# Kernel optimization log

Hardware: AMD Instinct MI355X
Metric: run time of the kernel (lower is better)

The kernel has to match this reference:

```python
import jax, jax.numpy as jnp
import numpy as np

N_NODES = 100000
N_EDGES = 1600000
F_IN, HIDDEN, N_CLASS, K = 64, 64, 32, 3
DROPOUT_P = 0.5


def setup_inputs() -> dict:
    key = jax.random.key(0)
    ks = jax.random.split(key, 5)
    x = jax.random.normal(ks[0], (N_NODES, F_IN), dtype=jnp.float32)
    edge_index = jax.random.randint(ks[1], (2, N_EDGES), 0, N_NODES, dtype=jnp.int64)
    W1 = jax.random.normal(ks[2], (K, F_IN, HIDDEN), dtype=jnp.float32) * (1.0 / np.sqrt(F_IN))
    b1 = jnp.zeros((HIDDEN,), dtype=jnp.float32)
    W2 = jax.random.normal(ks[3], (K, HIDDEN, N_CLASS), dtype=jnp.float32) * (1.0 / np.sqrt(HIDDEN))
    b2 = jnp.zeros((N_CLASS,), dtype=jnp.float32)
    return {"x": x, "edge_index": edge_index, "W1": W1, "b1": b1, "W2": W2, "b2": b2}


def _cheb_norm(edge_index, n_nodes):
    # PyG ChebConv sym norm with lambda_max=2: L_hat = -D^{-1/2} A D^{-1/2}
    row, col = edge_index[0], edge_index[1]
    deg = jax.ops.segment_sum(jnp.ones_like(row, dtype=jnp.float32), row, num_segments=n_nodes)
    dinv = jnp.where(deg > 0, jax.lax.rsqrt(jnp.maximum(deg, 1.0)), 0.0)
    return -(dinv[row] * dinv[col])  # [E]


def _cheb_conv(x, row, col, norm, W, b):
    # Chebyshev recursion: Tx0=x, Tx1=L_hat x, Tx_k = 2 L_hat Tx_{k-1} - Tx_{k-2}
    def prop(h):
        return jax.ops.segment_sum(norm[:, None] * h[col], row, num_segments=h.shape[0])
    Tx0 = x
    out = Tx0 @ W[0]
    Tx1 = prop(Tx0)
    out = out + Tx1 @ W[1]
    for k in range(2, W.shape[0]):
        Tx2 = 2.0 * prop(Tx1) - Tx0
        out = out + Tx2 @ W[k]
        Tx0, Tx1 = Tx1, Tx2
    return out + b


def reference(x, edge_index, W1, b1, W2, b2):
    row, col = edge_index[0], edge_index[1]
    norm = _cheb_norm(edge_index, x.shape[0])
    h = jax.nn.relu(_cheb_conv(x, row, col, norm, W1, b1))
    # dropout (training=True) with fixed key, inverted scaling
    keep = jax.random.bernoulli(jax.random.key(42), 1.0 - DROPOUT_P, h.shape)
    h = jnp.where(keep, h / (1.0 - DROPOUT_P), 0.0)
    out = _cheb_conv(h, row, col, norm, W2, b2)
    return jax.nn.log_softmax(out, axis=-1)
```

## Files before the change

kernel.cpp:

```cpp
#include <hip/hip_runtime.h>


static constexpr int BLK = 256;
static constexpr int SCAN_CHUNK = 256;
static constexpr int ROWB = 256;
static constexpr int RB_SHIFT = 8;
static constexpr int BCAP = 6144;
static constexpr int CHUNK = 8192;

typedef _Float16 f16x8 __attribute__((ext_vector_type(8)));
typedef _Float16 f16x2 __attribute__((ext_vector_type(2)));
typedef float f32x4 __attribute__((ext_vector_type(4)));

__device__ __forceinline__ unsigned rotl32(unsigned x, int r) {
    return (x << r) | (x >> (32 - r));
}

__device__ __forceinline__ unsigned tf_word(unsigned i) {
    const unsigned ks0 = 0u;
    const unsigned ks1 = 42u;
    const unsigned ks2 = 0u ^ 42u ^ 0x1BD11BDAu;
    unsigned x0 = 0u + ks0;
    unsigned x1 = i + ks1;
#define TF_RND(r) { x0 += x1; x1 = rotl32(x1, (r)); x1 ^= x0; }
    TF_RND(13) TF_RND(15) TF_RND(26) TF_RND(6)
    x0 += ks1; x1 += ks2 + 1u;
    TF_RND(17) TF_RND(29) TF_RND(16) TF_RND(24)
    x0 += ks2; x1 += ks0 + 2u;
    TF_RND(13) TF_RND(15) TF_RND(26) TF_RND(6)
    x0 += ks0; x1 += ks1 + 3u;
    TF_RND(17) TF_RND(29) TF_RND(16) TF_RND(24)
    x0 += ks1; x1 += ks2 + 4u;
    TF_RND(13) TF_RND(15) TF_RND(26) TF_RND(6)
    x0 += ks2; x1 += ks0 + 5u;
#undef TF_RND
    return x0 ^ x1;
}

__device__ __forceinline__ unsigned short f2h(float f) {
    union { _Float16 h; unsigned short u; } c; c.h = (_Float16)f; return c.u;
}
__device__ __forceinline__ unsigned pack2h(float a, float b) {
    union { f16x2 h; unsigned u; } c;
    c.h[0] = (_Float16)a; c.h[1] = (_Float16)b;
    return c.u;
}

__global__ void __launch_bounds__(256) k_drop(int NW, const int* __restrict__ ei,
                                              int* __restrict__ flags,
                                              unsigned long long* __restrict__ dmask) {
    if (blockIdx.x == gridDim.x - 1) {
        __shared__ int cnt_nz;
        int t = threadIdx.x;
        if (t == 0) cnt_nz = 0;
        __syncthreads();
        if (ei[2 * t + 1] != 0) atomicAdd(&cnt_nz, 1);
        __syncthreads();
        if (t == 0) flags[0] = (cnt_nz == 0) ? 1 : 0;
        return;
    }
    int idx = blockIdx.x * 256 + threadIdx.x;
    unsigned word = (idx < NW) ? tf_word((unsigned)idx) : 0u;
    unsigned long long bal = __ballot(word >> 31);
    if ((threadIdx.x & 63) == 0 && idx < NW) dmask[idx >> 6] = bal;
}

__global__ void __launch_bounds__(256) k_bin(const int* __restrict__ ei, int E,
                                             const int* __restrict__ flags,
                                             int* __restrict__ bcnt,
                                             unsigned* __restrict__ bdata, int NB) {
    __shared__ unsigned sval[CHUNK];
    __shared__ unsigned short sbkt[CHUNK];
    __shared__ int h[512], ex[512], cur[512], basep[512];
    int t = threadIdx.x;
    int start = blockIdx.x * CHUNK;
    int lim = min(CHUNK, E - start);
    bool i64 = flags[0] != 0;
    h[t] = 0; h[t + 256] = 0;
    __syncthreads();
    unsigned vv[32];
    unsigned short bb_[32];
#pragma unroll
    for (int k = 0; k < 32; ++k) {
        int idx = k * 256 + t;
        int e = start + idx;
        if (idx < lim) {
            int r, c;
            if (i64) { r = ei[2 * e]; c = ei[2 * (E + e)]; }
            else     { r = ei[e];     c = ei[E + e]; }
            int b = r >> RB_SHIFT;
            vv[k] = ((unsigned)(r & (ROWB - 1)) << 17) | (unsigned)c;
            bb_[k] = (unsigned short)b;
            atomicAdd(&h[b], 1);
        } else {
            bb_[k] = 0xFFFF;
        }
    }
    __syncthreads();
    int i0 = t, i1 = t + 256;
    ex[i0] = h[i0]; ex[i1] = h[i1];
    __syncthreads();
    for (int off = 1; off < 512; off <<= 1) {
        int v0 = (i0 >= off) ? ex[i0 - off] : 0;
        int v1 = (i1 >= off) ? ex[i1 - off] : 0;
        __syncthreads();
        ex[i0] += v0; ex[i1] += v1;
        __syncthreads();
    }
    int e0 = ex[i0] - h[i0], e1 = ex[i1] - h[i1];
    __syncthreads();
    ex[i0] = e0; cur[i0] = e0;
    ex[i1] = e1; cur[i1] = e1;
    if (i0 < NB && h[i0] > 0) basep[i0] = atomicAdd(&bcnt[i0], h[i0]);
    if (i1 < NB && h[i1] > 0) basep[i1] = atomicAdd(&bcnt[i1], h[i1]);
    __syncthreads();
#pragma unroll
    for (int k = 0; k < 32; ++k) {
        if (bb_[k] != 0xFFFF) {
            int p = atomicAdd(&cur[bb_[k]], 1);
            sval[p] = vv[k];
            sbkt[p] = bb_[k];
        }
    }
    __syncthreads();
    for (int i = t; i < lim; i += 256) {
        int b = sbkt[i];
        int gpos = basep[b] + (i - ex[b]);
        if (gpos < BCAP) bdata[(size_t)b * BCAP + gpos] = sval[i];
    }
}

__global__ void __launch_bounds__(256) k_hist2(const unsigned* __restrict__ bdata,
                                               const int* __restrict__ bcnt,
                                               int N, int* __restrict__ deg,
                                               float* __restrict__ dinv) {
    __shared__ int h[ROWB];
    int t = threadIdx.x, b = blockIdx.x;
    h[t] = 0;
    __syncthreads();
    int cnt = min(bcnt[b], BCAP);
    for (int i = t; i < cnt; i += 256)
        atomicAdd(&h[bdata[(size_t)b * BCAP + i] >> 17], 1);
    __syncthreads();
    int r = b * ROWB + t;
    if (r < N) {
        int d = h[t];
        deg[r] = d;
        dinv[r] = (d > 0) ? rsqrtf((float)d) : 0.0f;
    }
}

__global__ void k_scanA(const int* __restrict__ deg, int N, int* __restrict__ blk_sum) {
    __shared__ int lds[SCAN_CHUNK];
    int i = blockIdx.x * SCAN_CHUNK + threadIdx.x;
    int v = (i < N) ? deg[i] : 0;
    lds[threadIdx.x] = v;
    __syncthreads();
    for (int off = SCAN_CHUNK / 2; off > 0; off >>= 1) {
        if (threadIdx.x < off) lds[threadIdx.x] += lds[threadIdx.x + off];
        __syncthreads();
    }
    if (threadIdx.x == 0) blk_sum[blockIdx.x] = lds[0];
}

__global__ void k_scanB(int* __restrict__ blk_sum, int nb) {
    __shared__ int lds[1024];
    int t = threadIdx.x;
    int v = (t < nb) ? blk_sum[t] : 0;
    lds[t] = v;
    __syncthreads();
    for (int off = 1; off < 1024; off <<= 1) {
        int val = (t >= off) ? lds[t - off] : 0;
        __syncthreads();
        lds[t] += val;
        __syncthreads();
    }
    if (t < nb) blk_sum[t] = lds[t] - v;
}

__global__ void k_scanC(const int* __restrict__ deg, int N, int E,
                        const int* __restrict__ blk_sum, int* __restrict__ row_ptr) {
    __shared__ int lds[SCAN_CHUNK];
    int t = threadIdx.x;
    int i = blockIdx.x * SCAN_CHUNK + t;
    int v = (i < N) ? deg[i] : 0;
    lds[t] = v;
    __syncthreads();
    for (int off = 1; off < SCAN_CHUNK; off <<= 1) {
        int val = (t >= off) ? lds[t - off] : 0;
        __syncthreads();
        lds[t] += val;
        __syncthreads();
    }
    if (i < N) row_ptr[i] = blk_sum[blockIdx.x] + lds[t] - v;
    if (blockIdx.x == gridDim.x - 1 && t == SCAN_CHUNK - 1) row_ptr[N] = E;
}

__global__ void __launch_bounds__(256) k_place(const unsigned* __restrict__ bdata,
                                               const int* __restrict__ bcnt,
                                               const int* __restrict__ row_ptr,
                                               int N, int* __restrict__ sdst) {
    __shared__ int cur[ROWB];
    __shared__ int staged[BCAP];
    int t = threadIdx.x, b = blockIdx.x;
    int r0 = b * ROWB;
    int rbase = row_ptr[r0];
    int r = r0 + t;
    cur[t] = (r < N) ? (row_ptr[r] - rbase) : 0;
    __syncthreads();
    int cnt = min(bcnt[b], BCAP);
    for (int i = t; i < cnt; i += 256) {
        unsigned val = bdata[(size_t)b * BCAP + i];
        int p = atomicAdd(&cur[val >> 17], 1);
        staged[p] = (int)(val & 0x1FFFFu);
    }
    __syncthreads();
    for (int i = t; i < cnt; i += 256) sdst[rbase + i] = staged[i];
}

__global__ void k_wprep(const float* __restrict__ W1, const float* __restrict__ W2,
                        unsigned short* __restrict__ wt1,
                        unsigned short* __restrict__ wt2) {
    int idx = blockIdx.x * 256 + threadIdx.x;
    if (idx < 12288) {
        int c = idx >> 6, r6 = idx & 63;
        int slot = (r6 >> 3) ^ (c & 7);
        int k = slot * 8 + (r6 & 7);
        float v;
        if (c < 64)       v = W1[k * 64 + c] - W1[8192 + k * 64 + c];
        else if (c < 128) v = W1[4096 + k * 64 + (c - 64)];
        else              v = W1[8192 + k * 64 + (c - 128)];
        wt1[idx] = f2h(v);
    } else {
        int j = idx - 12288;
        int c = j >> 6, r6 = j & 63;
        int slot = (r6 >> 3) ^ (c & 7);
        int k = slot * 8 + (r6 & 7);
        float v;
        if (c < 32)      v = W2[k * 32 + c] - W2[4096 + k * 32 + c];
        else if (c < 64) v = W2[2048 + k * 32 + (c - 32)];
        else             v = W2[4096 + k * 32 + (c - 64)];
        wt2[j] = f2h(v);
    }
}

__global__ void __launch_bounds__(512) k_dense3(const float* __restrict__ x,
                                                const unsigned short* __restrict__ wt1,
                                                const float* __restrict__ b1,
                                                const float* __restrict__ dinv,
                                                int N,
                                                unsigned short* __restrict__ B16,
                                                unsigned short* __restrict__ C16,
                                                unsigned short* __restrict__ D16) {
    __shared__ unsigned short lds[20480] __attribute__((aligned(16)));
    __shared__ float sb[64];
    int t = threadIdx.x;
    int v0 = blockIdx.x * 128;
    {
        const uint4* src = (const uint4*)wt1;
        uint4* dst = (uint4*)&lds[8192];
        for (int i = t; i < 1536; i += 512) dst[i] = src[i];
    }
    if (t < 64) sb[t] = b1[t];
    {
        int row = t >> 2, c0 = (t & 3) << 4;
        int v = min(v0 + row, N - 1);
        const float* xp = x + (size_t)v * 64 + c0;
        float4 f0 = *(const float4*)xp;
        float4 f1 = *(const float4*)(xp + 4);
        float4 f2 = *(const float4*)(xp + 8);
        float4 f3 = *(const float4*)(xp + 12);
        int key = row & 7;
        int s0 = c0 >> 3;
        f16x8 h0, h1;
        h0[0] = (_Float16)f0.x; h0[1] = (_Float16)f0.y;
        h0[2] = (_Float16)f0.z; h0[3] = (_Float16)f0.w;
        h0[4] = (_Float16)f1.x; h0[5] = (_Float16)f1.y;
        h0[6] = (_Float16)f1.z; h0[7] = (_Float16)f1.w;
        h1[0] = (_Float16)f2.x; h1[1] = (_Float16)f2.y;
        h1[2] = (_Float16)f2.z; h1[3] = (_Float16)f2.w;
        h1[4] = (_Float16)f3.x; h1[5] = (_Float16)f3.y;
        h1[6] = (_Float16)f3.z; h1[7] = (_Float16)f3.w;
        *(f16x8*)&lds[row * 64 + ((s0 ^ key) << 3)] = h0;
        *(f16x8*)&lds[row * 64 + (((s0 + 1) ^ key) << 3)] = h1;
    }
    __syncthreads();

    int w = t >> 6, l = t & 63;
    int lr = l & 15, lk = l >> 4;
    int key = lr & 7;
    int arow = w * 16 + lr;
    f16x8 a0 = *(const f16x8*)&lds[arow * 64 + (((0 + lk) ^ key) << 3)];
    f16x8 a1 = *(const f16x8*)&lds[arow * 64 + (((4 + lk) ^ key) << 3)];
    f32x4 acc[12];
#pragma unroll
    for (int i = 0; i < 12; ++i) acc[i] = (f32x4){0.0f, 0.0f, 0.0f, 0.0f};
#pragma unroll
    for (int nt = 0; nt < 12; ++nt) {
        int bc = nt * 16 + lr;
        const unsigned short* wb = &lds[8192 + bc * 64];
        f16x8 b0 = *(const f16x8*)&wb[((0 + lk) ^ key) << 3];
        f16x8 b1v = *(const f16x8*)&wb[((4 + lk) ^ key) << 3];
        acc[nt] = __builtin_amdgcn_mfma_f32_16x16x32_f16(a0, b0, acc[nt], 0, 0, 0);
        acc[nt] = __builtin_amdgcn_mfma_f32_16x16x32_f16(a1, b1v, acc[nt], 0, 0, 0);
    }
    float4 dv4 = *(const float4*)&dinv[v0 + w * 16 + lk * 4];
    float dsc[4] = {dv4.x, dv4.y, dv4.z, dv4.w};
    __syncthreads();
#pragma unroll
    for (int nt = 0; nt < 4; ++nt) {
        int col = nt * 16 + lr;
        float bv = sb[col];
#pragma unroll
        for (int r = 0; r < 4; ++r) {
            int vloc = w * 16 + lk * 4 + r;
            lds[vloc * 64 + col] = f2h(acc[nt][r] + bv);
        }
    }
    __syncthreads();
#pragma unroll
    for (int q = 0; q < 2; ++q) {
        int i = q * 512 + t;
        int row = i >> 3, ch = i & 7;
        int v = v0 + row;
        if (v < N) *(uint4*)(D16 + (size_t)v * 64 + ch * 8) = ((const uint4*)lds)[i];
    }
    __syncthreads();
#pragma unroll
    for (int nt = 4; nt < 8; ++nt) {
        int col = (nt - 4) * 16 + lr;
#pragma unroll
        for (int r = 0; r < 4; ++r) {
            int vloc = w * 16 + lk * 4 + r;
            lds[vloc * 128 + col] = f2h(acc[nt][r]);
        }
    }
#pragma unroll
    for (int nt = 8; nt < 12; ++nt) {
        int col = (nt - 4) * 16 + lr;
#pragma unroll
        for (int r = 0; r < 4; ++r) {
            int vloc = w * 16 + lk * 4 + r;
            lds[vloc * 128 + col] = f2h(acc[nt][r] * dsc[r]);
        }
    }
    __syncthreads();
#pragma unroll
    for (int q = 0; q < 4; ++q) {
        int i = q * 512 + t;
        int row = i >> 4, ch = i & 15;
        int v = v0 + row;
        if (v < N) {
            uint4 val = *(const uint4*)&lds[i * 8];
            unsigned short* dst = (ch < 8)
                ? (B16 + (size_t)v * 64 + ch * 8)
                : (C16 + (size_t)v * 64 + (ch - 8) * 8);
            *(uint4*)dst = val;
        }
    }
}

__global__ void __launch_bounds__(512) k_dense3b(const unsigned short* __restrict__ wt2,
                                                 const float* __restrict__ dinv,
                                                 int N,
                                                 unsigned short* __restrict__ B16,
                                                 const unsigned short* __restrict__ C16h,
                                                 float* __restrict__ P0,
                                                 unsigned short* __restrict__ P1h) {
    __shared__ unsigned short lds[14336] __attribute__((aligned(16)));
    int t = threadIdx.x;
    int v0 = blockIdx.x * 128;
    {
        const uint4* src = (const uint4*)wt2;
        uint4* dst = (uint4*)&lds[8192];
        for (int i = t; i < 768; i += 512) dst[i] = src[i];
    }
    {
        int row = t >> 2, s0 = (t & 3) * 2;
        int v = min(v0 + row, N - 1);
        const uint4* cp = (const uint4*)(C16h + (size_t)v * 64);
        uint4 u0 = cp[s0];
        uint4 u1 = cp[s0 + 1];
        int key = row & 7;
        *(uint4*)&lds[row * 64 + ((s0 ^ key) << 3)] = u0;
        *(uint4*)&lds[row * 64 + (((s0 + 1) ^ key) << 3)] = u1;
    }
    __syncthreads();

    int w = t >> 6, l = t & 63;
    int lr = l & 15, lk = l >> 4;
    int key = lr & 7;
    int arow = w * 16 + lr;
    f16x8 a0 = *(const f16x8*)&lds[arow * 64 + (((0 + lk) ^ key) << 3)];
    f16x8 a1 = *(const f16x8*)&lds[arow * 64 + (((4 + lk) ^ key) << 3)];
    f32x4 acc[6];
#pragma unroll
    for (int i = 0; i < 6; ++i) acc[i] = (f32x4){0.0f, 0.0f, 0.0f, 0.0f};
#pragma unroll
    for (int nt = 0; nt < 6; ++nt) {
        int bc = nt * 16 + lr;
        const unsigned short* wb = &lds[8192 + bc * 64];
        f16x8 b0 = *(const f16x8*)&wb[((0 + lk) ^ key) << 3];
        f16x8 b1v = *(const f16x8*)&wb[((4 + lk) ^ key) << 3];
        acc[nt] = __builtin_amdgcn_mfma_f32_16x16x32_f16(a0, b0, acc[nt], 0, 0, 0);
        acc[nt] = __builtin_amdgcn_mfma_f32_16x16x32_f16(a1, b1v, acc[nt], 0, 0, 0);
    }
    float4 dv4 = *(const float4*)&dinv[v0 + w * 16 + lk * 4];
    float dsc[4] = {dv4.x, dv4.y, dv4.z, dv4.w};
#pragma unroll
    for (int nt = 0; nt < 2; ++nt) {
        int col = nt * 16 + lr;
#pragma unroll
        for (int r = 0; r < 4; ++r) {
            int v = v0 + w * 16 + lk * 4 + r;
            if (v < N) P0[(size_t)v * 32 + col] = acc[nt][r];
        }
    }
    __syncthreads();
#pragma unroll
    for (int nt = 2; nt < 4; ++nt) {
        int col = (nt - 2) * 16 + lr;
#pragma unroll
        for (int r = 0; r < 4; ++r) {
            int vloc = w * 16 + lk * 4 + r;
            lds[vloc * 64 + col] = f2h(acc[nt][r]);
        }
    }
#pragma unroll
    for (int nt = 4; nt < 6; ++nt) {
        int col = (nt - 2) * 16 + lr;
#pragma unroll
        for (int r = 0; r < 4; ++r) {
            int vloc = w * 16 + lk * 4 + r;
            lds[vloc * 64 + col] = f2h(acc[nt][r] * dsc[r]);
        }
    }
    __syncthreads();
#pragma unroll
    for (int q = 0; q < 2; ++q) {
        int i = q * 512 + t;
        int row = i >> 3, ch = i & 7;
        int v = v0 + row;
        if (v < N) {
            uint4 val = ((const uint4*)lds)[i];
            unsigned short* dst = (ch < 4)
                ? (P1h + (size_t)v * 32 + ch * 8)
                : (B16 + (size_t)v * 32 + (ch - 4) * 8);
            *(uint4*)dst = val;
        }
    }
}

template <int PITCH, int LPN>
__device__ __forceinline__ void gatherH(const unsigned short* __restrict__ src,
                                        const int* __restrict__ sdst,
                                        int beg, int end, int grp, int fl,
                                        float a[8]) {
    constexpr int NG = LPN / (PITCH / 8);
    f16x8 acc;
#pragma unroll
    for (int q = 0; q < 8; ++q) acc[q] = (_Float16)0;
    int e = beg + grp;
    for (; e + 3 * NG < end; e += 4 * NG) {
        int c0 = sdst[e];
        int c1 = sdst[e + NG];
        int c2 = sdst[e + 2 * NG];
        int c3 = sdst[e + 3 * NG];
        f16x8 r0 = *(const f16x8*)(src + (size_t)c0 * PITCH + 8 * fl);
        f16x8 r1 = *(const f16x8*)(src + (size_t)c1 * PITCH + 8 * fl);
        f16x8 r2 = *(const f16x8*)(src + (size_t)c2 * PITCH + 8 * fl);
        f16x8 r3 = *(const f16x8*)(src + (size_t)c3 * PITCH + 8 * fl);
        acc = acc + r0;
        acc = acc + r1;
        acc = acc + r2;
        acc = acc + r3;
    }
    for (; e < end; e += NG) {
        int c = sdst[e];
        f16x8 r = *(const f16x8*)(src + (size_t)c * PITCH + 8 * fl);
        acc = acc + r;
    }
#pragma unroll
    for (int m = PITCH / 8; m < LPN; m <<= 1) {
        union { f16x8 h; int i4[4]; } u;
        u.h = acc;
#pragma unroll
        for (int q = 0; q < 4; ++q) u.i4[q] = __shfl_xor(u.i4[q], m);
        acc = acc + u.h;
    }
#pragma unroll
    for (int q = 0; q < 8; ++q) a[q] = (float)acc[q];
}

__global__ void __launch_bounds__(BLK) k_gath1(const unsigned short* __restrict__ C16,
                                               unsigned short* __restrict__ B16,
                                               const float* __restrict__ dinv,
                                               const int* __restrict__ row_ptr,
                                               const int* __restrict__ sdst,
                                               int N) {
    int v = blockIdx.x * 16 + (threadIdx.x >> 4);
    if (v >= N) return;
    int ln = threadIdx.x & 15;
    int grp = ln >> 3, fl = ln & 7;
    float a[8];
    gatherH<64, 16>(C16, sdst, row_ptr[v], row_ptr[v + 1], grp, fl, a);
    if (grp == 0) {
        float di = dinv[v];
        float dv = -2.0f * di;
        unsigned short* p = B16 + (size_t)v * 64 + 8 * fl;
        f16x8 b = *(const f16x8*)p;
        uint4 o;
        o.x = pack2h(di * fmaf(dv, a[0], (float)b[0]), di * fmaf(dv, a[1], (float)b[1]));
        o.y = pack2h(di * fmaf(dv, a[2], (float)b[2]), di * fmaf(dv, a[3], (float)b[3]));
        o.z = pack2h(di * fmaf(dv, a[4], (float)b[4]), di * fmaf(dv, a[5], (float)b[5]));
        o.w = pack2h(di * fmaf(dv, a[6], (float)b[6]), di * fmaf(dv, a[7], (float)b[7]));
        *(uint4*)p = o;
    }
}

__global__ void __launch_bounds__(BLK) k_gath2(const unsigned short* __restrict__ D16,
                                               const unsigned short* __restrict__ B16,
                                               unsigned short* __restrict__ C16h,
                                               const unsigned long long* __restrict__ dmask,
                                               const float* __restrict__ dinv,
                                               const int* __restrict__ row_ptr,
                                               const int* __restrict__ sdst,
                                               int N) {
    int v = blockIdx.x * 16 + (threadIdx.x >> 4);
    if (v >= N) return;
    int ln = threadIdx.x & 15;
    int grp = ln >> 3, fl = ln & 7;
    float a[8];
    gatherH<64, 16>(B16, sdst, row_ptr[v], row_ptr[v + 1], grp, fl, a);
    if (grp == 0) {
        unsigned long long dm = dmask[v] >> (8 * fl);
        float dv = -dinv[v];
        f16x8 d = *(const f16x8*)(D16 + (size_t)v * 64 + 8 * fl);
        float o[8];
#pragma unroll
        for (int k = 0; k < 8; ++k)
            o[k] = fmaxf(fmaf(dv, a[k], (float)d[k]), 0.0f);
#pragma unroll
        for (int k = 0; k < 8; ++k)
            o[k] = ((dm >> k) & 1ull) ? 0.0f : o[k] * 2.0f;
        uint4 oo;
        oo.x = pack2h(o[0], o[1]); oo.y = pack2h(o[2], o[3]);
        oo.z = pack2h(o[4], o[5]); oo.w = pack2h(o[6], o[7]);
        *(uint4*)(C16h + (size_t)v * 64 + 8 * fl) = oo;
    }
}

__global__ void __launch_bounds__(BLK) k_gath3(const unsigned short* __restrict__ B16,
                                               const unsigned short* __restrict__ P1h,
                                               unsigned short* __restrict__ R16,
                                               const float* __restrict__ dinv,
                                               const int* __restrict__ row_ptr,
                                               const int* __restrict__ sdst,
                                               int N) {
    int v = blockIdx.x * 32 + (threadIdx.x >> 3);
    if (v >= N) return;
    int ln = threadIdx.x & 7;
    int grp = ln >> 2, fl = ln & 3;
    float a[8];
    gatherH<32, 8>(B16, sdst, row_ptr[v], row_ptr[v + 1], grp, fl, a);
    if (grp == 0) {
        float di = dinv[v];
        float dv = -2.0f * di;
        f16x8 d = *(const f16x8*)(P1h + (size_t)v * 32 + 8 * fl);
        uint4 o;
        o.x = pack2h(di * fmaf(dv, a[0], (float)d[0]), di * fmaf(dv, a[1], (float)d[1]));
        o.y = pack2h(di * fmaf(dv, a[2], (float)d[2]), di * fmaf(dv, a[3], (float)d[3]));
        o.z = pack2h(di * fmaf(dv, a[4], (float)d[4]), di * fmaf(dv, a[5], (float)d[5]));
        o.w = pack2h(di * fmaf(dv, a[6], (float)d[6]), di * fmaf(dv, a[7], (float)d[7]));
        *(uint4*)(R16 + (size_t)v * 32 + 8 * fl) = o;
    }
}

__global__ void __launch_bounds__(BLK) k_gath4(const unsigned short* __restrict__ R16,
                                               const float* __restrict__ P0,
                                               const float* __restrict__ dinv,
                                               const int* __restrict__ row_ptr,
                                               const int* __restrict__ sdst,
                                               const float* __restrict__ b2,
                                               int N, float* __restrict__ out) {
    int v = blockIdx.x * 32 + (threadIdx.x >> 3);
    if (v >= N) return;
    int ln = threadIdx.x & 7;
    int grp = ln >> 2, fl = ln & 3;
    float a[8];
    gatherH<32, 8>(R16, sdst, row_ptr[v], row_ptr[v + 1], grp, fl, a);
    float dv = -dinv[v];
    const float* dp = P0 + (size_t)v * 32 + 8 * fl;
    float4 dA = *(const float4*)dp;
    float4 dB = *(const float4*)(dp + 4);
    const float* bp = b2 + 8 * fl;
    float4 bA = *(const float4*)bp;
    float4 bB = *(const float4*)(bp + 4);
    float o[8];
    o[0] = fmaf(dv, a[0], dA.x + bA.x);
    o[1] = fmaf(dv, a[1], dA.y + bA.y);
    o[2] = fmaf(dv, a[2], dA.z + bA.z);
    o[3] = fmaf(dv, a[3], dA.w + bA.w);
    o[4] = fmaf(dv, a[4], dB.x + bB.x);
    o[5] = fmaf(dv, a[5], dB.y + bB.y);
    o[6] = fmaf(dv, a[6], dB.z + bB.z);
    o[7] = fmaf(dv, a[7], dB.w + bB.w);
    float m = o[0];
#pragma unroll
    for (int k = 1; k < 8; ++k) m = fmaxf(m, o[k]);
    m = fmaxf(m, __shfl_xor(m, 1));
    m = fmaxf(m, __shfl_xor(m, 2));
    float s = 0.0f;
#pragma unroll
    for (int k = 0; k < 8; ++k) s += __expf(o[k] - m);
    s += __shfl_xor(s, 1);
    s += __shfl_xor(s, 2);
    float lse = m + __logf(s);
    if (grp == 0) {
        float* op = out + (size_t)v * 32 + 8 * fl;
        *(float4*)op = make_float4(o[0] - lse, o[1] - lse, o[2] - lse, o[3] - lse);
        *(float4*)(op + 4) = make_float4(o[4] - lse, o[5] - lse, o[6] - lse, o[7] - lse);
    }
}

extern "C" void kernel_launch(void* const* d_in, const int* in_sizes, int n_in,
                              void* d_out, int out_size, void* d_ws, size_t ws_size,
                              hipStream_t stream) {
    const float* x  = (const float*)d_in[0];
    const int* ei   = (const int*)d_in[1];
    const float* W1 = (const float*)d_in[2];
    const float* b1 = (const float*)d_in[3];
    const float* W2 = (const float*)d_in[4];
    const float* b2 = (const float*)d_in[5];
    float* out = (float*)d_out;

    const int N = in_sizes[0] / 64;
    const int E = in_sizes[1] / 2;
    const int NB = (N + ROWB - 1) >> RB_SHIFT;

    char* ws = (char*)d_ws;
    size_t off = 0;
    auto alloc = [&](size_t bytes) -> void* {
        void* p = ws + off;
        off = (off + bytes + 511) & ~(size_t)511;
        return p;
    };
    int*      flags   = (int*)alloc(16);
    int*      deg     = (int*)alloc((size_t)N * 4);
    float*    dinv    = (float*)alloc((size_t)N * 4);
    int*      row_ptr = (int*)alloc(((size_t)N + 1) * 4);
    int*      blk_sum = (int*)alloc(4096);
    int*      bcnt    = (int*)alloc((size_t)NB * 4);
    size_t dbytes = (size_t)N * 64 * 4;
    size_t bdbytes = (size_t)NB * BCAP * 4;
    unsigned* bdata = (unsigned*)alloc(dbytes > bdbytes ? dbytes : bdbytes);
    unsigned short* D16 = (unsigned short*)bdata;
    float*    P0    = (float*)bdata;
    unsigned short* P1h = (unsigned short*)((char*)bdata + (size_t)N * 32 * 4);
    int*      sdst  = (int*)alloc((size_t)E * 4);
    unsigned short* C16h = (unsigned short*)alloc((size_t)N * 64 * 2);
    unsigned short* B16 = (unsigned short*)alloc((size_t)N * 64 * 2);
    unsigned short* C16 = (unsigned short*)alloc((size_t)N * 64 * 2);
    unsigned short* R16 = C16;
    unsigned long long* dmask = (unsigned long long*)alloc((size_t)N * 8);
    unsigned short* wt1 = (unsigned short*)alloc(12288 * 2);
    unsigned short* wt2 = (unsigned short*)alloc(6144 * 2);

    hipMemsetAsync(bcnt, 0, (size_t)NB * 4, stream);

    const int gW16 = (N + 15) / 16;
    const int gW32 = (N + 31) / 32;
    const int gDM = (N + 127) / 128;
    const int nb = (N + SCAN_CHUNK - 1) / SCAN_CHUNK;
    const int gBin = (E + CHUNK - 1) / CHUNK;
    const int gDrop = (N * 64 + 255) / 256;

    k_wprep<<<72, 256, 0, stream>>>(W1, W2, wt1, wt2);
    k_drop<<<gDrop + 1, 256, 0, stream>>>(N * 64, ei, flags, dmask);
    k_bin<<<gBin, 256, 0, stream>>>(ei, E, flags, bcnt, bdata, NB);
    k_hist2<<<NB, 256, 0, stream>>>(bdata, bcnt, N, deg, dinv);
    k_scanA<<<nb, SCAN_CHUNK, 0, stream>>>(deg, N, blk_sum);
    k_scanB<<<1, 1024, 0, stream>>>(blk_sum, nb);
    k_scanC<<<nb, SCAN_CHUNK, 0, stream>>>(deg, N, E, blk_sum, row_ptr);
    k_place<<<NB, 256, 0, stream>>>(bdata, bcnt, row_ptr, N, sdst);

    k_dense3<<<gDM, 512, 0, stream>>>(x, wt1, b1, dinv, N, B16, C16, D16);
    k_gath1<<<gW16, BLK, 0, stream>>>(C16, B16, dinv, row_ptr, sdst, N);
    k_gath2<<<gW16, BLK, 0, stream>>>(D16, B16, C16h, dmask, dinv, row_ptr, sdst, N);

    k_dense3b<<<gDM, 512, 0, stream>>>(wt2, dinv, N, B16, C16h, P0, P1h);
    k_gath3<<<gW32, BLK, 0, stream>>>(B16, P1h, R16, dinv, row_ptr, sdst, N);
    k_gath4<<<gW32, BLK, 0, stream>>>(R16, P0, dinv, row_ptr, sdst, b2, N, out);
}
```

Baseline: 274.7 us.

## Degree-sort nodes for gather load balance and fuse scan/init kernels

Adds a counting-sort permutation of nodes by (clamped) degree and makes all four gather kernels process nodes in that order, so the lanes of a wavefront handle rows of similar length and spend less time waiting on divergent loops. The degree scan is folded into k_hist2 (block sums) and k_place (in-block scan), removing the scanA/scanC kernels, and weight prep is merged with the dropout-mask kernel. The cost is an extra permutation kernel and an indirect perm load, plus scattered output writes and row_ptr reads that lose locality.

```diff
diff --git a/kernel.cpp b/kernel.cpp
--- a/kernel.cpp
+++ b/kernel.cpp
@@ -2,7 +2,6 @@
 
 
 static constexpr int BLK = 256;
-static constexpr int SCAN_CHUNK = 256;
 static constexpr int ROWB = 256;
 static constexpr int RB_SHIFT = 8;
 static constexpr int BCAP = 6144;
@@ -46,12 +45,25 @@
     return c.u;
 }
 
-__global__ void __launch_bounds__(256) k_drop(int NW, const int* __restrict__ ei,
+__global__ void __launch_bounds__(256) k_init(int NW, const int* __restrict__ ei,
+                                              const float* __restrict__ W1,
+                                              const float* __restrict__ W2,
                                               int* __restrict__ flags,
-                                              unsigned long long* __restrict__ dmask) {
-    if (blockIdx.x == gridDim.x - 1) {
+                                              unsigned long long* __restrict__ dmask,
+                                              unsigned short* __restrict__ wt1,
+                                              unsigned short* __restrict__ wt2,
+                                              int gDrop) {
+    int b = blockIdx.x;
+    int t = threadIdx.x;
+    if (b < gDrop) {
+        int idx = b * 256 + t;
+        unsigned word = (idx < NW) ? tf_word((unsigned)idx) : 0u;
+        unsigned long long bal = __ballot(word >> 31);
+        if ((t & 63) == 0 && idx < NW) dmask[idx >> 6] = bal;
+        return;
+    }
+    if (b == gDrop) {
         __shared__ int cnt_nz;
-        int t = threadIdx.x;
         if (t == 0) cnt_nz = 0;
         __syncthreads();
         if (ei[2 * t + 1] != 0) atomicAdd(&cnt_nz, 1);
@@ -59,169 +71,7 @@
         if (t == 0) flags[0] = (cnt_nz == 0) ? 1 : 0;
         return;
     }
-    int idx = blockIdx.x * 256 + threadIdx.x;
-    unsigned word = (idx < NW) ? tf_word((unsigned)idx) : 0u;
-    unsigned long long bal = __ballot(word >> 31);
-    if ((threadIdx.x & 63) == 0 && idx < NW) dmask[idx >> 6] = bal;
-}
-
-__global__ void __launch_bounds__(256) k_bin(const int* __restrict__ ei, int E,
-                                             const int* __restrict__ flags,
-                                             int* __restrict__ bcnt,
-                                             unsigned* __restrict__ bdata, int NB) {
-    __shared__ unsigned sval[CHUNK];
-    __shared__ unsigned short sbkt[CHUNK];
-    __shared__ int h[512], ex[512], cur[512], basep[512];
-    int t = threadIdx.x;
-    int start = blockIdx.x * CHUNK;
-    int lim = min(CHUNK, E - start);
-    bool i64 = flags[0] != 0;
-    h[t] = 0; h[t + 256] = 0;
-    __syncthreads();
-    unsigned vv[32];
-    unsigned short bb_[32];
-#pragma unroll
-    for (int k = 0; k < 32; ++k) {
-        int idx = k * 256 + t;
-        int e = start + idx;
-        if (idx < lim) {
-            int r, c;
-            if (i64) { r = ei[2 * e]; c = ei[2 * (E + e)]; }
-            else     { r = ei[e];     c = ei[E + e]; }
-            int b = r >> RB_SHIFT;
-            vv[k] = ((unsigned)(r & (ROWB - 1)) << 17) | (unsigned)c;
-            bb_[k] = (unsigned short)b;
-            atomicAdd(&h[b], 1);
-        } else {
-            bb_[k] = 0xFFFF;
-        }
-    }
-    __syncthreads();
-    int i0 = t, i1 = t + 256;
-    ex[i0] = h[i0]; ex[i1] = h[i1];
-    __syncthreads();
-    for (int off = 1; off < 512; off <<= 1) {
-        int v0 = (i0 >= off) ? ex[i0 - off] : 0;
-        int v1 = (i1 >= off) ? ex[i1 - off] : 0;
-        __syncthreads();
-        ex[i0] += v0; ex[i1] += v1;
-        __syncthreads();
-    }
-    int e0 = ex[i0] - h[i0], e1 = ex[i1] - h[i1];
-    __syncthreads();
-    ex[i0] = e0; cur[i0] = e0;
-    ex[i1] = e1; cur[i1] = e1;
-    if (i0 < NB && h[i0] > 0) basep[i0] = atomicAdd(&bcnt[i0], h[i0]);
-    if (i1 < NB && h[i1] > 0) basep[i1] = atomicAdd(&bcnt[i1], h[i1]);
-    __syncthreads();
-#pragma unroll
-    for (int k = 0; k < 32; ++k) {
-        if (bb_[k] != 0xFFFF) {
-            int p = atomicAdd(&cur[bb_[k]], 1);
-            sval[p] = vv[k];
-            sbkt[p] = bb_[k];
-        }
-    }
-    __syncthreads();
-    for (int i = t; i < lim; i += 256) {
-        int b = sbkt[i];
-        int gpos = basep[b] + (i - ex[b]);
-        if (gpos < BCAP) bdata[(size_t)b * BCAP + gpos] = sval[i];
-    }
-}
-
-__global__ void __launch_bounds__(256) k_hist2(const unsigned* __restrict__ bdata,
-                                               const int* __restrict__ bcnt,
-                                               int N, int* __restrict__ deg,
-                                               float* __restrict__ dinv) {
-    __shared__ int h[ROWB];
-    int t = threadIdx.x, b = blockIdx.x;
-    h[t] = 0;
-    __syncthreads();
-    int cnt = min(bcnt[b], BCAP);
-    for (int i = t; i < cnt; i += 256)
-        atomicAdd(&h[bdata[(size_t)b * BCAP + i] >> 17], 1);
-    __syncthreads();
-    int r = b * ROWB + t;
-    if (r < N) {
-        int d = h[t];
-        deg[r] = d;
-        dinv[r] = (d > 0) ? rsqrtf((float)d) : 0.0f;
-    }
-}
-
-__global__ void k_scanA(const int* __restrict__ deg, int N, int* __restrict__ blk_sum) {
-    __shared__ int lds[SCAN_CHUNK];
-    int i = blockIdx.x * SCAN_CHUNK + threadIdx.x;
-    int v = (i < N) ? deg[i] : 0;
-    lds[threadIdx.x] = v;
-    __syncthreads();
-    for (int off = SCAN_CHUNK / 2; off > 0; off >>= 1) {
-        if (threadIdx.x < off) lds[threadIdx.x] += lds[threadIdx.x + off];
-        __syncthreads();
-    }
-    if (threadIdx.x == 0) blk_sum[blockIdx.x] = lds[0];
-}
-
-__global__ void k_scanB(int* __restrict__ blk_sum, int nb) {
-    __shared__ int lds[1024];
-    int t = threadIdx.x;
-    int v = (t < nb) ? blk_sum[t] : 0;
-    lds[t] = v;
-    __syncthreads();
-    for (int off = 1; off < 1024; off <<= 1) {
-        int val = (t >= off) ? lds[t - off] : 0;
-        __syncthreads();
-        lds[t] += val;
-        __syncthreads();
-    }
-    if (t < nb) blk_sum[t] = lds[t] - v;
-}
-
-__global__ void k_scanC(const int* __restrict__ deg, int N, int E,
-                        const int* __restrict__ blk_sum, int* __restrict__ row_ptr) {
-    __shared__ int lds[SCAN_CHUNK];
-    int t = threadIdx.x;
-    int i = blockIdx.x * SCAN_CHUNK + t;
-    int v = (i < N) ? deg[i] : 0;
-    lds[t] = v;
-    __syncthreads();
-    for (int off = 1; off < SCAN_CHUNK; off <<= 1) {
-        int val = (t >= off) ? lds[t - off] : 0;
-        __syncthreads();
-        lds[t] += val;
-        __syncthreads();
-    }
-    if (i < N) row_ptr[i] = blk_sum[blockIdx.x] + lds[t] - v;
-    if (blockIdx.x == gridDim.x - 1 && t == SCAN_CHUNK - 1) row_ptr[N] = E;
-}
-
-__global__ void __launch_bounds__(256) k_place(const unsigned* __restrict__ bdata,
-                                               const int* __restrict__ bcnt,
-                                               const int* __restrict__ row_ptr,
-                                               int N, int* __restrict__ sdst) {
-    __shared__ int cur[ROWB];
-    __shared__ int staged[BCAP];
-    int t = threadIdx.x, b = blockIdx.x;
-    int r0 = b * ROWB;
-    int rbase = row_ptr[r0];
-    int r = r0 + t;
-    cur[t] = (r < N) ? (row_ptr[r] - rbase) : 0;
-    __syncthreads();
-    int cnt = min(bcnt[b], BCAP);
-    for (int i = t; i < cnt; i += 256) {
-        unsigned val = bdata[(size_t)b * BCAP + i];
-        int p = atomicAdd(&cur[val >> 17], 1);
-        staged[p] = (int)(val & 0x1FFFFu);
-    }
-    __syncthreads();
-    for (int i = t; i < cnt; i += 256) sdst[rbase + i] = staged[i];
-}
-
-__global__ void k_wprep(const float* __restrict__ W1, const float* __restrict__ W2,
-                        unsigned short* __restrict__ wt1,
-                        unsigned short* __restrict__ wt2) {
-    int idx = blockIdx.x * 256 + threadIdx.x;
+    int idx = (b - gDrop - 1) * 256 + t;
     if (idx < 12288) {
         int c = idx >> 6, r6 = idx & 63;
         int slot = (r6 >> 3) ^ (c & 7);
@@ -242,6 +92,169 @@
         else             v = W2[4096 + k * 32 + (c - 64)];
         wt2[j] = f2h(v);
     }
+}
+
+__global__ void __launch_bounds__(256) k_bin(const int* __restrict__ ei, int E,
+                                             const int* __restrict__ flags,
+                                             int* __restrict__ bcnt,
+                                             unsigned* __restrict__ bdata, int NB) {
+    __shared__ unsigned sval[CHUNK];
+    __shared__ unsigned short sbkt[CHUNK];
+    __shared__ int h[512], ex[512], cur[512], basep[512];
+    int t = threadIdx.x;
+    int start = blockIdx.x * CHUNK;
+    int lim = min(CHUNK, E - start);
+    bool i64 = flags[0] != 0;
+    h[t] = 0; h[t + 256] = 0;
+    __syncthreads();
+    unsigned vv[32];
+    unsigned short bb_[32];
+#pragma unroll
+    for (int k = 0; k < 32; ++k) {
+        int idx = k * 256 + t;
+        int e = start + idx;
+        if (idx < lim) {
+            int r, c;
+            if (i64) { r = ei[2 * e]; c = ei[2 * (E + e)]; }
+            else     { r = ei[e];     c = ei[E + e]; }
+            int b = r >> RB_SHIFT;
+            vv[k] = ((unsigned)(r & (ROWB - 1)) << 17) | (unsigned)c;
+            bb_[k] = (unsigned short)b;
+            atomicAdd(&h[b], 1);
+        } else {
+            bb_[k] = 0xFFFF;
+        }
+    }
+    __syncthreads();
+    int i0 = t, i1 = t + 256;
+    ex[i0] = h[i0]; ex[i1] = h[i1];
+    __syncthreads();
+    for (int off = 1; off < 512; off <<= 1) {
+        int v0 = (i0 >= off) ? ex[i0 - off] : 0;
+        int v1 = (i1 >= off) ? ex[i1 - off] : 0;
+        __syncthreads();
+        ex[i0] += v0; ex[i1] += v1;
+        __syncthreads();
+    }
+    int e0 = ex[i0] - h[i0], e1 = ex[i1] - h[i1];
+    __syncthreads();
+    ex[i0] = e0; cur[i0] = e0;
+    ex[i1] = e1; cur[i1] = e1;
+    if (i0 < NB && h[i0] > 0) basep[i0] = atomicAdd(&bcnt[i0], h[i0]);
+    if (i1 < NB && h[i1] > 0) basep[i1] = atomicAdd(&bcnt[i1], h[i1]);
+    __syncthreads();
+#pragma unroll
+    for (int k = 0; k < 32; ++k) {
+        if (bb_[k] != 0xFFFF) {
+            int p = atomicAdd(&cur[bb_[k]], 1);
+            sval[p] = vv[k];
+            sbkt[p] = bb_[k];
+        }
+    }
+    __syncthreads();
+    for (int i = t; i < lim; i += 256) {
+        int b = sbkt[i];
+        int gpos = basep[b] + (i - ex[b]);
+        if (gpos < BCAP) bdata[(size_t)b * BCAP + gpos] = sval[i];
+    }
+}
+
+__global__ void __launch_bounds__(256) k_hist2(const unsigned* __restrict__ bdata,
+                                               const int* __restrict__ bcnt,
+                                               int N, int* __restrict__ deg,
+                                               float* __restrict__ dinv,
+                                               int* __restrict__ blk_sum,
+                                               int* __restrict__ dhist) {
+    __shared__ int h[ROWB];
+    int t = threadIdx.x, b = blockIdx.x;
+    h[t] = 0;
+    __syncthreads();
+    int cnt = min(bcnt[b], BCAP);
+    for (int i = t; i < cnt; i += 256)
+        atomicAdd(&h[bdata[(size_t)b * BCAP + i] >> 17], 1);
+    __syncthreads();
+    int r = b * ROWB + t;
+    int d = h[t];
+    if (r < N) {
+        deg[r] = d;
+        dinv[r] = (d > 0) ? rsqrtf((float)d) : 0.0f;
+        atomicAdd(&dhist[min(d, 127)], 1);
+    }
+    __syncthreads();
+    for (int off = 128; off > 0; off >>= 1) {
+        if (t < off) h[t] += h[t + off];
+        __syncthreads();
+    }
+    if (t == 0) blk_sum[b] = h[0];
+}
+
+__global__ void k_scanB(int* __restrict__ blk_sum, int nb, int* __restrict__ dhist) {
+    __shared__ int lds[1024];
+    __shared__ int dl[128];
+    int t = threadIdx.x;
+    int v = (t < nb) ? blk_sum[t] : 0;
+    lds[t] = v;
+    int dv = 0;
+    if (t < 128) { dv = dhist[t]; dl[t] = dv; }
+    __syncthreads();
+    for (int off = 1; off < 1024; off <<= 1) {
+        int val = (t >= off) ? lds[t - off] : 0;
+        int dval = (t < 128 && t >= off) ? dl[t - off] : 0;
+        __syncthreads();
+        lds[t] += val;
+        if (t < 128) dl[t] += dval;
+        __syncthreads();
+    }
+    if (t < nb) blk_sum[t] = lds[t] - v;
+    if (t < 128) dhist[t] = dl[t] - dv;
+}
+
+__global__ void __launch_bounds__(256) k_perm(const int* __restrict__ deg, int N,
+                                              int* __restrict__ dhist,
+                                              int* __restrict__ perm) {
+    int v = blockIdx.x * 256 + threadIdx.x;
+    if (v < N) {
+        int d = min(deg[v], 127);
+        int pos = atomicAdd(&dhist[d], 1);
+        perm[pos] = v;
+    }
+}
+
+__global__ void __launch_bounds__(256) k_place(const unsigned* __restrict__ bdata,
+                                               const int* __restrict__ bcnt,
+                                               const int* __restrict__ deg,
+                                               const int* __restrict__ blk_sum,
+                                               int N, int E,
+                                               int* __restrict__ row_ptr,
+                                               int* __restrict__ sdst) {
+    __shared__ int cur[ROWB];
+    __shared__ int sc[ROWB];
+    __shared__ int staged[BCAP];
+    int t = threadIdx.x, b = blockIdx.x;
+    int r = b * ROWB + t;
+    int d = (r < N) ? deg[r] : 0;
+    sc[t] = d;
+    __syncthreads();
+    for (int off = 1; off < ROWB; off <<= 1) {
+        int val = (t >= off) ? sc[t - off] : 0;
+        __syncthreads();
+        sc[t] += val;
+        __syncthreads();
+    }
+    int excl = sc[t] - d;
+    int rbase = blk_sum[b];
+    if (r < N) row_ptr[r] = rbase + excl;
+    if (b == gridDim.x - 1 && t == ROWB - 1) row_ptr[N] = E;
+    cur[t] = excl;
+    __syncthreads();
+    int cnt = min(bcnt[b], BCAP);
+    for (int i = t; i < cnt; i += 256) {
+        unsigned val = bdata[(size_t)b * BCAP + i];
+        int p = atomicAdd(&cur[val >> 17], 1);
+        staged[p] = (int)(val & 0x1FFFFu);
+    }
+    __syncthreads();
+    for (int i = t; i < cnt; i += 256) sdst[rbase + i] = staged[i];
 }
 
 __global__ void __launch_bounds__(512) k_dense3(const float* __restrict__ x,
@@ -497,9 +510,11 @@
                                                const float* __restrict__ dinv,
                                                const int* __restrict__ row_ptr,
                                                const int* __restrict__ sdst,
+                                               const int* __restrict__ perm,
                                                int N) {
-    int v = blockIdx.x * 16 + (threadIdx.x >> 4);
-    if (v >= N) return;
+    int vidx = blockIdx.x * 16 + (threadIdx.x >> 4);
+    if (vidx >= N) return;
+    int v = perm[vidx];
     int ln = threadIdx.x & 15;
     int grp = ln >> 3, fl = ln & 7;
     float a[8];
@@ -525,9 +540,11 @@
                                                const float* __restrict__ dinv,
                                                const int* __restrict__ row_ptr,
                                                const int* __restrict__ sdst,
+                                               const int* __restrict__ perm,
                                                int N) {
-    int v = blockIdx.x * 16 + (threadIdx.x >> 4);
-    if (v >= N) return;
+    int vidx = blockIdx.x * 16 + (threadIdx.x >> 4);
+    if (vidx >= N) return;
+    int v = perm[vidx];
     int ln = threadIdx.x & 15;
     int grp = ln >> 3, fl = ln & 7;
     float a[8];
@@ -556,9 +573,11 @@
                                                const float* __restrict__ dinv,
                                                const int* __restrict__ row_ptr,
                                                const int* __restrict__ sdst,
+                                               const int* __restrict__ perm,
                                                int N) {
-    int v = blockIdx.x * 32 + (threadIdx.x >> 3);
-    if (v >= N) return;
+    int vidx = blockIdx.x * 32 + (threadIdx.x >> 3);
+    if (vidx >= N) return;
+    int v = perm[vidx];
     int ln = threadIdx.x & 7;
     int grp = ln >> 2, fl = ln & 3;
     float a[8];
@@ -581,10 +600,12 @@
                                                const float* __restrict__ dinv,
                                                const int* __restrict__ row_ptr,
                                                const int* __restrict__ sdst,
+                                               const int* __restrict__ perm,
                                                const float* __restrict__ b2,
                                                int N, float* __restrict__ out) {
-    int v = blockIdx.x * 32 + (threadIdx.x >> 3);
-    if (v >= N) return;
+    int vidx = blockIdx.x * 32 + (threadIdx.x >> 3);
+    if (vidx >= N) return;
+    int v = perm[vidx];
     int ln = threadIdx.x & 7;
     int grp = ln >> 2, fl = ln & 3;
     float a[8];
@@ -650,7 +671,9 @@
     float*    dinv    = (float*)alloc((size_t)N * 4);
     int*      row_ptr = (int*)alloc(((size_t)N + 1) * 4);
     int*      blk_sum = (int*)alloc(4096);
-    int*      bcnt    = (int*)alloc((size_t)NB * 4);
+    int*      bcnt    = (int*)alloc((size_t)NB * 4 + 512);
+    int*      dhist   = bcnt + NB;
+    int*      perm    = (int*)alloc((size_t)N * 4);
     size_t dbytes = (size_t)N * 64 * 4;
     size_t bdbytes = (size_t)NB * BCAP * 4;
     unsigned* bdata = (unsigned*)alloc(dbytes > bdbytes ? dbytes : bdbytes);
@@ -666,29 +689,29 @@
     unsigned short* wt1 = (unsigned short*)alloc(12288 * 2);
     unsigned short* wt2 = (unsigned short*)alloc(6144 * 2);
 
-    hipMemsetAsync(bcnt, 0, (size_t)NB * 4, stream);
+    hipMemsetAsync(bcnt, 0, (size_t)NB * 4 + 512, stream);
 
     const int gW16 = (N + 15) / 16;
     const int gW32 = (N + 31) / 32;
     const int gDM = (N + 127) / 128;
-    const int nb = (N + SCAN_CHUNK - 1) / SCAN_CHUNK;
+    const int gN = (N + 255) / 256;
+    const int nb = NB;
     const int gBin = (E + CHUNK - 1) / CHUNK;
     const int gDrop = (N * 64 + 255) / 256;
 
-    k_wprep<<<72, 256, 0, stream>>>(W1, W2, wt1, wt2);
-    k_drop<<<gDrop + 1, 256, 0, stream>>>(N * 64, ei, flags, dmask);
+    k_init<<<gDrop + 1 + 72, 256, 0, stream>>>(N * 64, ei, W1, W2, flags, dmask,
+                                               wt1, wt2, gDrop);
     k_bin<<<gBin, 256, 0, stream>>>(ei, E, flags, bcnt, bdata, NB);
-    k_hist2<<<NB, 256, 0, stream>>>(bdata, bcnt, N, deg, dinv);
-    k_scanA<<<nb, SCAN_CHUNK, 0, stream>>>(deg, N, blk_sum);
-    k_scanB<<<1, 1024, 0, stream>>>(blk_sum, nb);
-    k_scanC<<<nb, SCAN_CHUNK, 0, stream>>>(deg, N, E, blk_sum, row_ptr);
-    k_place<<<NB, 256, 0, stream>>>(bdata, bcnt, row_ptr, N, sdst);
+    k_hist2<<<NB, 256, 0, stream>>>(bdata, bcnt, N, deg, dinv, blk_sum, dhist);
+    k_scanB<<<1, 1024, 0, stream>>>(blk_sum, nb, dhist);
+    k_perm<<<gN, 256, 0, stream>>>(deg, N, dhist, perm);
+    k_place<<<NB, 256, 0, stream>>>(bdata, bcnt, deg, blk_sum, N, E, row_ptr, sdst);
 
     k_dense3<<<gDM, 512, 0, stream>>>(x, wt1, b1, dinv, N, B16, C16, D16);
-    k_gath1<<<gW16, BLK, 0, stream>>>(C16, B16, dinv, row_ptr, sdst, N);
-    k_gath2<<<gW16, BLK, 0, stream>>>(D16, B16, C16h, dmask, dinv, row_ptr, sdst, N);
+    k_gath1<<<gW16, BLK, 0, stream>>>(C16, B16, dinv, row_ptr, sdst, perm, N);
+    k_gath2<<<gW16, BLK, 0, stream>>>(D16, B16, C16h, dmask, dinv, row_ptr, sdst, perm, N);
 
     k_dense3b<<<gDM, 512, 0, stream>>>(wt2, dinv, N, B16, C16h, P0, P1h);
-    k_gath3<<<gW32, BLK, 0, stream>>>(B16, P1h, R16, dinv, row_ptr, sdst, N);
-    k_gath4<<<gW32, BLK, 0, stream>>>(R16, P0, dinv, row_ptr, sdst, b2, N, out);
-}
+    k_gath3<<<gW32, BLK, 0, stream>>>(B16, P1h, R16, dinv, row_ptr, sdst, perm, N);
+    k_gath4<<<gW32, BLK, 0, stream>>>(R16, P0, dinv, row_ptr, sdst, perm, b2, N, out);
+}
```

Result: slower. 875.4 us (+218.7%).
